# Optimization experiments

Hardware: AMD Instinct MI355X
Metric: run time of the kernel (lower is better)

Reference implementation:

```python
import jax, jax.numpy as jnp
import numpy as np

D_S = 1024
N_HEADS = 16
HEAD_DIM = D_S // N_HEADS
FFN_DIM = 4096
B, S = 2, 1024
LN_EPS = 1e-5


def _layernorm(x, gamma, beta):
    mu = jnp.mean(x, axis=-1, keepdims=True)
    var = jnp.var(x, axis=-1, keepdims=True)
    return (x - mu) * jax.lax.rsqrt(var + LN_EPS) * gamma + beta


def _mish(x):
    return x * jnp.tanh(jax.nn.softplus(x))


def setup_inputs() -> dict:
    key = jax.random.key(0)
    ks = jax.random.split(key, 12)
    std = 1.0 / np.sqrt(D_S)
    return {
        "x": jax.random.normal(ks[0], (B, S, D_S), jnp.float32),
        "attn_bias": jax.random.normal(ks[1], (B, N_HEADS, S, S), jnp.float32),
        "ln1_g": jnp.ones((D_S,), jnp.float32),
        "ln1_b": jnp.zeros((D_S,), jnp.float32),
        "Wqkv": jax.random.normal(ks[2], (D_S, 3 * D_S), jnp.float32) * std,
        "bqkv": jax.random.normal(ks[3], (3 * D_S,), jnp.float32) * 0.02,
        "Wo": jax.random.normal(ks[4], (D_S, D_S), jnp.float32) * std,
        "bo": jax.random.normal(ks[5], (D_S,), jnp.float32) * 0.02,
        "ln2_g": jnp.ones((D_S,), jnp.float32),
        "ln2_b": jnp.zeros((D_S,), jnp.float32),
        "W1": jax.random.normal(ks[6], (D_S, FFN_DIM), jnp.float32) * std,
        "b1": jax.random.normal(ks[7], (FFN_DIM,), jnp.float32) * 0.02,
        "W2": jax.random.normal(ks[8], (FFN_DIM, D_S), jnp.float32) * (1.0 / np.sqrt(FFN_DIM)),
        "b2": jax.random.normal(ks[9], (D_S,), jnp.float32) * 0.02,
    }


def reference(x, attn_bias, ln1_g, ln1_b, Wqkv, bqkv, Wo, bo, ln2_g, ln2_b, W1, b1, W2, b2):
    b, s, d = x.shape
    h = _layernorm(x, ln1_g, ln1_b)
    qkv = (h @ Wqkv + bqkv).reshape(b, s, 3, N_HEADS, HEAD_DIM)
    q, k, v = qkv[:, :, 0], qkv[:, :, 1], qkv[:, :, 2]  # [B,S,H,hd]
    scale = HEAD_DIM ** -0.5
    # scores: [B,H,S,S]
    scores = jnp.einsum("bqhd,bkhd->bhqk", q, k) * scale + attn_bias
    attn = jax.nn.softmax(scores, axis=-1)
    ctx = jnp.einsum("bhqk,bkhd->bqhd", attn, v).reshape(b, s, d)
    x = x + (ctx @ Wo + bo)
    h2 = _layernorm(x, ln2_g, ln2_b)
    ffn = _mish(h2 @ W1 + b1) @ W2 + b2
    return x + ffn
```

## Files before the change

### kernel.cpp

```cpp
#include <hip/hip_runtime.h>


typedef __attribute__((ext_vector_type(8))) __bf16 bf16x8;
typedef __attribute__((ext_vector_type(4))) float  f32x4;

__device__ __forceinline__ unsigned short f2bf(float f) {
  unsigned int u = __builtin_bit_cast(unsigned int, f);
  u += 0x7fffu + ((u >> 16) & 1u);
  return (unsigned short)(u >> 16);
}

__device__ __forceinline__ void gload16(const void* g, void* l) {
  __builtin_amdgcn_global_load_lds(
      (const __attribute__((address_space(1))) void*)g,
      (__attribute__((address_space(3))) void*)l, 16, 0, 0);
}

__global__ void convert_all(const float* __restrict__ Wqkv, const float* __restrict__ Wo,
                            const float* __restrict__ W1, const float* __restrict__ W2,
                            unsigned short* __restrict__ wqkv_t, unsigned short* __restrict__ wo_t,
                            unsigned short* __restrict__ w1_t, unsigned short* __restrict__ w2_t) {
  const int id = blockIdx.x;
  const float* W; unsigned short* Wt; int K, N, t;
  if (id < 3072)      { W = Wqkv; Wt = wqkv_t; K = 1024; N = 3072; t = id; }
  else if (id < 4096) { W = Wo;   Wt = wo_t;   K = 1024; N = 1024; t = id - 3072; }
  else if (id < 8192) { W = W1;   Wt = w1_t;   K = 1024; N = 4096; t = id - 4096; }
  else                { W = W2;   Wt = w2_t;   K = 4096; N = 1024; t = id - 8192; }
  const int nx = N >> 5;
  const int n0 = (t % nx) * 32, k0 = (t / nx) * 32;

  __shared__ float tile[32][33];
  const int tx = threadIdx.x, ty = threadIdx.y;
#pragma unroll
  for (int r = 0; r < 4; ++r)
    tile[ty + 8 * r][tx] = W[(size_t)(k0 + ty + 8 * r) * N + n0 + tx];
  __syncthreads();
#pragma unroll
  for (int r = 0; r < 4; ++r)
    Wt[(size_t)(n0 + ty + 8 * r) * K + k0 + tx] = f2bf(tile[tx][ty + 8 * r]);
}

__global__ __launch_bounds__(256) void ln_kernel(const float* __restrict__ in,
                                                 const float* __restrict__ g,
                                                 const float* __restrict__ b,
                                                 unsigned short* __restrict__ out) {
  const int row = blockIdx.x;
  const int t = threadIdx.x;
  const float4 v = reinterpret_cast<const float4*>(in + (size_t)row * 1024)[t];
  float s  = v.x + v.y + v.z + v.w;
  float s2 = v.x * v.x + v.y * v.y + v.z * v.z + v.w * v.w;
#pragma unroll
  for (int m = 1; m < 64; m <<= 1) { s += __shfl_xor(s, m); s2 += __shfl_xor(s2, m); }
  __shared__ float ps[4], ps2[4];
  const int wv = t >> 6;
  if ((t & 63) == 0) { ps[wv] = s; ps2[wv] = s2; }
  __syncthreads();
  float ts = 0.f, ts2 = 0.f;
#pragma unroll
  for (int i = 0; i < 4; ++i) { ts += ps[i]; ts2 += ps2[i]; }
  const float mu = ts * (1.f / 1024.f);
  const float var = ts2 * (1.f / 1024.f) - mu * mu;
  const float rstd = rsqrtf(var + 1e-5f);
  const float4 gg = reinterpret_cast<const float4*>(g)[t];
  const float4 bb = reinterpret_cast<const float4*>(b)[t];
  ushort4 ov;
  ov.x = f2bf((v.x - mu) * rstd * gg.x + bb.x);
  ov.y = f2bf((v.y - mu) * rstd * gg.y + bb.y);
  ov.z = f2bf((v.z - mu) * rstd * gg.z + bb.z);
  ov.w = f2bf((v.w - mu) * rstd * gg.w + bb.w);
  *reinterpret_cast<ushort4*>(out + (size_t)row * 1024 + t * 4) = ov;
}

template <int MODE, int BM, int BN>
__global__ __launch_bounds__(256, 2) void gemm_kernel(
    const unsigned short* __restrict__ A, const unsigned short* __restrict__ Bt,
    const float* __restrict__ bias, int M, int N, int K,
    float* __restrict__ outf, const float* __restrict__ res,
    unsigned short* __restrict__ outb,
    unsigned short* __restrict__ kbuf, unsigned short* __restrict__ vtbuf) {
  constexpr int BK = 64;
  constexpr int WN = (BN >= 128 || BM == 64) ? 2 : 1;
  constexpr int WM = 4 / WN;
  constexpr int WR = BM / WM / 16;
  constexpr int WC = BN / WN / 16;
  constexpr int AI = BM / 32, BI = BN / 32;
  __shared__ unsigned short a_sh[2][BM * BK];
  __shared__ unsigned short b_sh[2][BN * BK];

  const int tid = threadIdx.x;
  const int wave = tid >> 6, lane = tid & 63;
  const int wm = wave / WN, wn = wave % WN;
  const int l15 = lane & 15, l4 = lane >> 4;

  const int nwg = gridDim.x, cpx = nwg >> 3;
  const int swz = (blockIdx.x & 7) * cpx + (blockIdx.x >> 3);
  const int GY = M / BM;
  const long bm0 = (long)(swz % GY) * BM;
  const long bn0 = (long)(swz / GY) * BN;

  const int sr8 = lane >> 3;
  const int gc  = ((lane & 7) ^ sr8) * 8;

  const unsigned short* agp[AI];
  const unsigned short* bgp[BI];
  int aoff[AI], boff[BI];
#pragma unroll
  for (int i = 0; i < AI; ++i) {
    const int r = wave * (BM / 4) + i * 8;
    agp[i] = A + (bm0 + r + sr8) * (long)K + gc;
    aoff[i] = r * BK;
  }
#pragma unroll
  for (int i = 0; i < BI; ++i) {
    const int r = wave * (BN / 4) + i * 8;
    bgp[i] = Bt + (bn0 + r + sr8) * (long)K + gc;
    boff[i] = r * BK;
  }

  auto stage = [&](int buf, int k0) {
#pragma unroll
    for (int i = 0; i < AI; ++i) gload16(agp[i] + k0, &a_sh[buf][aoff[i]]);
#pragma unroll
    for (int i = 0; i < BI; ++i) gload16(bgp[i] + k0, &b_sh[buf][boff[i]]);
  };

  f32x4 acc[WR][WC] = {};

  stage(0, 0);
  asm volatile("s_waitcnt vmcnt(0)" ::: "memory");
  __syncthreads();

  const int NT = K / BK;
  for (int t = 0; t < NT; ++t) {
    const int cur = t & 1;
    if (t + 1 < NT) stage(cur ^ 1, (t + 1) * BK);

#pragma unroll
    for (int kk = 0; kk < 2; ++kk) {
      bf16x8 af[WR], bfr[WC];
#pragma unroll
      for (int mf = 0; mf < WR; ++mf) {
        const int r = wm * (BM / WM) + mf * 16 + l15;
        const int c = ((kk * 4 + l4) ^ (r & 7)) * 8;
        af[mf] = *reinterpret_cast<const bf16x8*>(&a_sh[cur][r * BK + c]);
      }
#pragma unroll
      for (int nf = 0; nf < WC; ++nf) {
        const int r = wn * (BN / WN) + nf * 16 + l15;
        const int c = ((kk * 4 + l4) ^ (r & 7)) * 8;
        bfr[nf] = *reinterpret_cast<const bf16x8*>(&b_sh[cur][r * BK + c]);
      }
#pragma unroll
      for (int mf = 0; mf < WR; ++mf)
#pragma unroll
        for (int nf = 0; nf < WC; ++nf)
          acc[mf][nf] = __builtin_amdgcn_mfma_f32_16x16x32_bf16(af[mf], bfr[nf], acc[mf][nf], 0, 0, 0);
    }

    asm volatile("s_waitcnt vmcnt(0)" ::: "memory");
    __syncthreads();
  }

#pragma unroll
  for (int mf = 0; mf < WR; ++mf) {
#pragma unroll
    for (int nf = 0; nf < WC; ++nf) {
#pragma unroll
      for (int r = 0; r < 4; ++r) {
        const long row = bm0 + wm * (BM / WM) + mf * 16 + 4 * l4 + r;
        const long col = bn0 + wn * (BN / WN) + nf * 16 + l15;
        float v = acc[mf][nf][r] + bias[col];
        if constexpr (MODE == 0) {
          const int n = (int)col;
          const int which = n >> 10, rem = n & 1023;
          const int head = rem >> 6, d = rem & 63;
          const int b = (int)(row >> 10), s = (int)(row & 1023);
          const unsigned short bv = f2bf(v);
          const long qi = ((long)(b * 16 + head) * 1024 + s) * 64 + d;
          if (which == 0)      outb[qi] = bv;
          else if (which == 1) kbuf[qi] = bv;
          else                 vtbuf[((long)(b * 16 + head) * 64 + d) * 1024 + s] = bv;
        } else if constexpr (MODE == 1) {
          outf[row * N + col] = v + res[row * N + col];
        } else if constexpr (MODE == 2) {
          float mv;
          if (v > 20.f) mv = v;
          else { const float t2 = __expf(v); const float u = t2 * t2 + 2.f * t2;
                 mv = v * u / (u + 2.f); }
          outb[row * (long)N + col] = f2bf(mv);
        } else {
          outf[row * N + col] = v + res[row * N + col];
        }
      }
    }
  }
}

__global__ __launch_bounds__(512, 2) void attn_kernel(
    const unsigned short* __restrict__ qb, const unsigned short* __restrict__ kb,
    const unsigned short* __restrict__ vtb, const float* __restrict__ bias,
    unsigned short* __restrict__ ctx) {
  constexpr int S = 1024;
  __shared__ unsigned short k_sh[2][64 * 64];
  __shared__ unsigned short vt_sh[2][64 * 64];
  __shared__ unsigned short p_sh[8][16 * 72];

  const int bh = blockIdx.y;
  const int q0 = blockIdx.x * 128;
  const int tid = threadIdx.x, wave = tid >> 6, lane = tid & 63;
  const int l15 = lane & 15, l4 = lane >> 4;

  const long qbase = ((long)bh * S + q0 + wave * 16 + l15) * 64;
  const bf16x8 qf0 = *reinterpret_cast<const bf16x8*>(qb + qbase + 8 * l4);
  const bf16x8 qf1 = *reinterpret_cast<const bf16x8*>(qb + qbase + 8 * l4 + 32);

  const int sr8 = lane >> 3;
  const int gchunk = ((lane & 7) ^ sr8) * 8;
  const long kbase = (long)bh * S * 64;
  const long vbase = (long)bh * 64 * S;

  const float* bB = bias + ((long)bh * S + q0 + wave * 16 + 4 * l4) * S + l15;

  f32x4 oacc[4] = {};
  float lacc[4] = {};
  float ba[4][4], bb2[4][4];

  auto stageKV = [&](int kv, int buf) {
    const int r = wave * 8;
    gload16(kb + kbase + (long)(kv + r + sr8) * 64 + gchunk, &k_sh[buf][r * 64]);
    gload16(vtb + vbase + (long)(r + sr8) * S + kv + gchunk, &vt_sh[buf][r * 64]);
  };

  stageKV(0, 0);
#pragma unroll
  for (int r = 0; r < 4; ++r)
#pragma unroll
    for (int nf = 0; nf < 4; ++nf)
      ba[r][nf] = bB[(long)r * S + nf * 16];
  asm volatile("s_waitcnt vmcnt(0)" ::: "memory");
  __syncthreads();

#pragma unroll 1
  for (int tt = 0; tt < 8; ++tt) {
    const int t0 = 2 * tt;
#pragma unroll
    for (int half = 0; half < 2; ++half) {
      const int t = t0 + half;
      const int cur = half, nxt = half ^ 1;
      float (*bcur)[4] = half ? bb2 : ba;
      float (*bnxt)[4] = half ? ba : bb2;

      if (t < 15) stageKV((t + 1) * 64, nxt);

      f32x4 sc[4];
#pragma unroll
      for (int nf = 0; nf < 4; ++nf) {
        const int r = nf * 16 + l15;
        const bf16x8 kf0 = *reinterpret_cast<const bf16x8*>(
            &k_sh[cur][r * 64 + ((l4) ^ (r & 7)) * 8]);
        const bf16x8 kf1 = *reinterpret_cast<const bf16x8*>(
            &k_sh[cur][r * 64 + ((l4 + 4) ^ (r & 7)) * 8]);
        f32x4 z = {};
        z = __builtin_amdgcn_mfma_f32_16x16x32_bf16(qf0, kf0, z, 0, 0, 0);
        sc[nf] = __builtin_amdgcn_mfma_f32_16x16x32_bf16(qf1, kf1, z, 0, 0, 0);
      }

      if (t < 15) {
        const float* bn = bB + (t + 1) * 64;
#pragma unroll
        for (int r = 0; r < 4; ++r)
#pragma unroll
          for (int nf = 0; nf < 4; ++nf)
            bnxt[r][nf] = bn[(long)r * S + nf * 16];
      }

      float pv[4][4];
#pragma unroll
      for (int r = 0; r < 4; ++r) {
        float ls = 0.f;
#pragma unroll
        for (int nf = 0; nf < 4; ++nf) {
          const float p = __expf(sc[nf][r] * 0.125f + bcur[r][nf]);
          pv[nf][r] = p;
          ls += p;
        }
        lacc[r] += ls;
      }

#pragma unroll
      for (int nf = 0; nf < 4; ++nf)
#pragma unroll
        for (int r = 0; r < 4; ++r)
          p_sh[wave][(4 * l4 + r) * 72 + nf * 16 + l15] = f2bf(pv[nf][r]);

      const bf16x8 pa0 = *reinterpret_cast<const bf16x8*>(&p_sh[wave][l15 * 72 + 8 * l4]);
      const bf16x8 pa1 = *reinterpret_cast<const bf16x8*>(&p_sh[wave][l15 * 72 + 8 * l4 + 32]);
#pragma unroll
      for (int nf = 0; nf < 4; ++nf) {
        const int r = nf * 16 + l15;
        const bf16x8 vf0 = *reinterpret_cast<const bf16x8*>(
            &vt_sh[cur][r * 64 + ((l4) ^ (r & 7)) * 8]);
        const bf16x8 vf1 = *reinterpret_cast<const bf16x8*>(
            &vt_sh[cur][r * 64 + ((l4 + 4) ^ (r & 7)) * 8]);
        oacc[nf] = __builtin_amdgcn_mfma_f32_16x16x32_bf16(pa0, vf0, oacc[nf], 0, 0, 0);
        oacc[nf] = __builtin_amdgcn_mfma_f32_16x16x32_bf16(pa1, vf1, oacc[nf], 0, 0, 0);
      }

      asm volatile("s_waitcnt vmcnt(0)" ::: "memory");
      __syncthreads();
    }
  }

#pragma unroll
  for (int r = 0; r < 4; ++r) {
    float v = lacc[r];
    v += __shfl_xor(v, 1);
    v += __shfl_xor(v, 2);
    v += __shfl_xor(v, 4);
    v += __shfl_xor(v, 8);
    lacc[r] = 1.f / v;
  }

  const int b = bh >> 4, h = bh & 15;
#pragma unroll
  for (int nf = 0; nf < 4; ++nf)
#pragma unroll
    for (int r = 0; r < 4; ++r) {
      const long s = q0 + wave * 16 + 4 * l4 + r;
      const long col = h * 64 + nf * 16 + l15;
      ctx[((long)b * S + s) * 1024 + col] = f2bf(oacc[nf][r] * lacc[r]);
    }
}

extern "C" void kernel_launch(void* const* d_in, const int* in_sizes, int n_in,
                              void* d_out, int out_size, void* d_ws, size_t ws_size,
                              hipStream_t stream) {
  const float* x    = (const float*)d_in[0];
  const float* ab   = (const float*)d_in[1];
  const float* ln1g = (const float*)d_in[2];
  const float* ln1b = (const float*)d_in[3];
  const float* Wqkv = (const float*)d_in[4];
  const float* bqkv = (const float*)d_in[5];
  const float* Wo   = (const float*)d_in[6];
  const float* bo   = (const float*)d_in[7];
  const float* ln2g = (const float*)d_in[8];
  const float* ln2b = (const float*)d_in[9];
  const float* W1   = (const float*)d_in[10];
  const float* b1   = (const float*)d_in[11];
  const float* W2   = (const float*)d_in[12];
  const float* b2   = (const float*)d_in[13];
  float* out = (float*)d_out;

  char* ws = (char*)d_ws;
  size_t off = 0;
  auto alloc = [&](size_t bytes) {
    char* p = ws + off;
    off += (bytes + 255) & ~(size_t)255;
    return p;
  };
  unsigned short* wqkv_t = (unsigned short*)alloc((size_t)3072 * 1024 * 2);
  unsigned short* wo_t   = (unsigned short*)alloc((size_t)1024 * 1024 * 2);
  unsigned short* w1_t   = (unsigned short*)alloc((size_t)4096 * 1024 * 2);
  unsigned short* w2_t   = (unsigned short*)alloc((size_t)4096 * 1024 * 2);
  unsigned short* h1     = (unsigned short*)alloc((size_t)2048 * 1024 * 2);
  unsigned short* qbuf   = (unsigned short*)alloc((size_t)2048 * 1024 * 2);
  unsigned short* kbuf   = (unsigned short*)alloc((size_t)2048 * 1024 * 2);
  unsigned short* vtbuf  = (unsigned short*)alloc((size_t)2048 * 1024 * 2);
  unsigned short* ctx    = (unsigned short*)alloc((size_t)2048 * 1024 * 2);
  unsigned short* h2     = (unsigned short*)alloc((size_t)2048 * 1024 * 2);
  float*          r1     = (float*)alloc((size_t)2048 * 1024 * 4);
  unsigned short* ffn1   = h1;
  (void)ws_size; (void)in_sizes; (void)n_in; (void)out_size;

  convert_all<<<12288, dim3(32, 8), 0, stream>>>(Wqkv, Wo, W1, W2,
                                                 wqkv_t, wo_t, w1_t, w2_t);

  ln_kernel<<<2048, 256, 0, stream>>>(x, ln1g, ln1b, h1);

  gemm_kernel<0, 128, 128><<<384, 256, 0, stream>>>(h1, wqkv_t, bqkv, 2048, 3072, 1024,
                                                    nullptr, nullptr, qbuf, kbuf, vtbuf);

  attn_kernel<<<dim3(8, 32), 512, 0, stream>>>(qbuf, kbuf, vtbuf, ab, ctx);

  gemm_kernel<1, 64, 64><<<512, 256, 0, stream>>>(ctx, wo_t, bo, 2048, 1024, 1024,
                                                  r1, x, nullptr, nullptr, nullptr);

  ln_kernel<<<2048, 256, 0, stream>>>(r1, ln2g, ln2b, h2);

  gemm_kernel<2, 128, 128><<<512, 256, 0, stream>>>(h2, w1_t, b1, 2048, 4096, 1024,
                                                    nullptr, nullptr, ffn1, nullptr, nullptr);

  gemm_kernel<3, 64, 64><<<512, 256, 0, stream>>>(ffn1, w2_t, b2, 2048, 1024, 4096,
                                                  out, r1, nullptr, nullptr, nullptr);
}
```

Measured before the change: 178.4 us.

## Triple-buffer GEMM, use 8 waves for 128 tiles, fuse LN1 into convert

New measurement: 193.0 us. +8.2%, slower.

```diff
diff --git a/kernel.cpp b/kernel.cpp
--- a/kernel.cpp
+++ b/kernel.cpp
@@ -16,28 +16,60 @@
       (__attribute__((address_space(3))) void*)l, 16, 0, 0);
 }
 
-__global__ void convert_all(const float* __restrict__ Wqkv, const float* __restrict__ Wo,
-                            const float* __restrict__ W1, const float* __restrict__ W2,
-                            unsigned short* __restrict__ wqkv_t, unsigned short* __restrict__ wo_t,
-                            unsigned short* __restrict__ w1_t, unsigned short* __restrict__ w2_t) {
+__global__ __launch_bounds__(256) void convert_ln(
+    const float* __restrict__ Wqkv, const float* __restrict__ Wo,
+    const float* __restrict__ W1, const float* __restrict__ W2,
+    const float* __restrict__ x, const float* __restrict__ g,
+    const float* __restrict__ bln,
+    unsigned short* __restrict__ wqkv_t, unsigned short* __restrict__ wo_t,
+    unsigned short* __restrict__ w1_t, unsigned short* __restrict__ w2_t,
+    unsigned short* __restrict__ h1) {
+  __shared__ float tile[32][33];
+  __shared__ float ps[4], ps2[4];
   const int id = blockIdx.x;
-  const float* W; unsigned short* Wt; int K, N, t;
-  if (id < 3072)      { W = Wqkv; Wt = wqkv_t; K = 1024; N = 3072; t = id; }
-  else if (id < 4096) { W = Wo;   Wt = wo_t;   K = 1024; N = 1024; t = id - 3072; }
-  else if (id < 8192) { W = W1;   Wt = w1_t;   K = 1024; N = 4096; t = id - 4096; }
-  else                { W = W2;   Wt = w2_t;   K = 4096; N = 1024; t = id - 8192; }
-  const int nx = N >> 5;
-  const int n0 = (t % nx) * 32, k0 = (t / nx) * 32;
-
-  __shared__ float tile[32][33];
   const int tx = threadIdx.x, ty = threadIdx.y;
-#pragma unroll
-  for (int r = 0; r < 4; ++r)
-    tile[ty + 8 * r][tx] = W[(size_t)(k0 + ty + 8 * r) * N + n0 + tx];
-  __syncthreads();
-#pragma unroll
-  for (int r = 0; r < 4; ++r)
-    Wt[(size_t)(n0 + ty + 8 * r) * K + k0 + tx] = f2bf(tile[tx][ty + 8 * r]);
+
+  if (id < 12288) {
+    const float* W; unsigned short* Wt; int K, N, t;
+    if (id < 3072)      { W = Wqkv; Wt = wqkv_t; K = 1024; N = 3072; t = id; }
+    else if (id < 4096) { W = Wo;   Wt = wo_t;   K = 1024; N = 1024; t = id - 3072; }
+    else if (id < 8192) { W = W1;   Wt = w1_t;   K = 1024; N = 4096; t = id - 4096; }
+    else                { W = W2;   Wt = w2_t;   K = 4096; N = 1024; t = id - 8192; }
+    const int nx = N >> 5;
+    const int n0 = (t % nx) * 32, k0 = (t / nx) * 32;
+#pragma unroll
+    for (int r = 0; r < 4; ++r)
+      tile[ty + 8 * r][tx] = W[(size_t)(k0 + ty + 8 * r) * N + n0 + tx];
+    __syncthreads();
+#pragma unroll
+    for (int r = 0; r < 4; ++r)
+      Wt[(size_t)(n0 + ty + 8 * r) * K + k0 + tx] = f2bf(tile[tx][ty + 8 * r]);
+  } else {
+    const int row = id - 12288;
+    const int t = ty * 32 + tx;
+    const float4 v = reinterpret_cast<const float4*>(x + (size_t)row * 1024)[t];
+    float s  = v.x + v.y + v.z + v.w;
+    float s2 = v.x * v.x + v.y * v.y + v.z * v.z + v.w * v.w;
+#pragma unroll
+    for (int m = 1; m < 64; m <<= 1) { s += __shfl_xor(s, m); s2 += __shfl_xor(s2, m); }
+    const int wv = t >> 6;
+    if ((t & 63) == 0) { ps[wv] = s; ps2[wv] = s2; }
+    __syncthreads();
+    float ts = 0.f, ts2 = 0.f;
+#pragma unroll
+    for (int i = 0; i < 4; ++i) { ts += ps[i]; ts2 += ps2[i]; }
+    const float mu = ts * (1.f / 1024.f);
+    const float var = ts2 * (1.f / 1024.f) - mu * mu;
+    const float rstd = rsqrtf(var + 1e-5f);
+    const float4 gg = reinterpret_cast<const float4*>(g)[t];
+    const float4 bb = reinterpret_cast<const float4*>(bln)[t];
+    ushort4 ov;
+    ov.x = f2bf((v.x - mu) * rstd * gg.x + bb.x);
+    ov.y = f2bf((v.y - mu) * rstd * gg.y + bb.y);
+    ov.z = f2bf((v.z - mu) * rstd * gg.z + bb.z);
+    ov.w = f2bf((v.w - mu) * rstd * gg.w + bb.w);
+    *reinterpret_cast<ushort4*>(h1 + (size_t)row * 1024 + t * 4) = ov;
+  }
 }
 
 __global__ __launch_bounds__(256) void ln_kernel(const float* __restrict__ in,
@@ -72,24 +104,24 @@
 }
 
 template <int MODE, int BM, int BN>
-__global__ __launch_bounds__(256, 2) void gemm_kernel(
+__global__ __launch_bounds__(BM == 128 ? 512 : 256, BM == 128 ? 2 : 3)
+void gemm_kernel(
     const unsigned short* __restrict__ A, const unsigned short* __restrict__ Bt,
     const float* __restrict__ bias, int M, int N, int K,
     float* __restrict__ outf, const float* __restrict__ res,
     unsigned short* __restrict__ outb,
     unsigned short* __restrict__ kbuf, unsigned short* __restrict__ vtbuf) {
   constexpr int BK = 64;
-  constexpr int WN = (BN >= 128 || BM == 64) ? 2 : 1;
-  constexpr int WM = 4 / WN;
-  constexpr int WR = BM / WM / 16;
-  constexpr int WC = BN / WN / 16;
-  constexpr int AI = BM / 32, BI = BN / 32;
-  __shared__ unsigned short a_sh[2][BM * BK];
-  __shared__ unsigned short b_sh[2][BN * BK];
+  constexpr int NW  = (BM == 128) ? 8 : 4;
+  constexpr int WNG = NW / 2;
+  constexpr int WR  = BM / 32;
+  constexpr int WC  = 2;
+  __shared__ unsigned short a_sh[3][BM * BK];
+  __shared__ unsigned short b_sh[3][BN * BK];
 
   const int tid = threadIdx.x;
   const int wave = tid >> 6, lane = tid & 63;
-  const int wm = wave / WN, wn = wave % WN;
+  const int wm = wave / WNG, wn = wave % WNG;
   const int l15 = lane & 15, l4 = lane >> 4;
 
   const int nwg = gridDim.x, cpx = nwg >> 3;
@@ -101,52 +133,50 @@
   const int sr8 = lane >> 3;
   const int gc  = ((lane & 7) ^ sr8) * 8;
 
-  const unsigned short* agp[AI];
-  const unsigned short* bgp[BI];
-  int aoff[AI], boff[BI];
-#pragma unroll
-  for (int i = 0; i < AI; ++i) {
-    const int r = wave * (BM / 4) + i * 8;
+  const unsigned short* agp[2];
+  const unsigned short* bgp[2];
+  int aoff[2], boff[2];
+#pragma unroll
+  for (int i = 0; i < 2; ++i) {
+    const int r = (wave * 2 + i) * 8;
     agp[i] = A + (bm0 + r + sr8) * (long)K + gc;
     aoff[i] = r * BK;
-  }
-#pragma unroll
-  for (int i = 0; i < BI; ++i) {
-    const int r = wave * (BN / 4) + i * 8;
     bgp[i] = Bt + (bn0 + r + sr8) * (long)K + gc;
     boff[i] = r * BK;
   }
 
   auto stage = [&](int buf, int k0) {
 #pragma unroll
-    for (int i = 0; i < AI; ++i) gload16(agp[i] + k0, &a_sh[buf][aoff[i]]);
-#pragma unroll
-    for (int i = 0; i < BI; ++i) gload16(bgp[i] + k0, &b_sh[buf][boff[i]]);
+    for (int i = 0; i < 2; ++i) gload16(agp[i] + k0, &a_sh[buf][aoff[i]]);
+#pragma unroll
+    for (int i = 0; i < 2; ++i) gload16(bgp[i] + k0, &b_sh[buf][boff[i]]);
   };
 
   f32x4 acc[WR][WC] = {};
+  const int NT = K / BK;
 
   stage(0, 0);
-  asm volatile("s_waitcnt vmcnt(0)" ::: "memory");
+  stage(1, BK);
+  asm volatile("s_waitcnt vmcnt(4)" ::: "memory");
   __syncthreads();
 
-  const int NT = K / BK;
   for (int t = 0; t < NT; ++t) {
-    const int cur = t & 1;
-    if (t + 1 < NT) stage(cur ^ 1, (t + 1) * BK);
+    const int cur = t % 3;
+    const bool pf = (t + 2 < NT);
+    if (pf) stage((t + 2) % 3, (t + 2) * BK);
 
 #pragma unroll
     for (int kk = 0; kk < 2; ++kk) {
       bf16x8 af[WR], bfr[WC];
 #pragma unroll
       for (int mf = 0; mf < WR; ++mf) {
-        const int r = wm * (BM / WM) + mf * 16 + l15;
+        const int r = wm * (BM / 2) + mf * 16 + l15;
         const int c = ((kk * 4 + l4) ^ (r & 7)) * 8;
         af[mf] = *reinterpret_cast<const bf16x8*>(&a_sh[cur][r * BK + c]);
       }
 #pragma unroll
       for (int nf = 0; nf < WC; ++nf) {
-        const int r = wn * (BN / WN) + nf * 16 + l15;
+        const int r = wn * 32 + nf * 16 + l15;
         const int c = ((kk * 4 + l4) ^ (r & 7)) * 8;
         bfr[nf] = *reinterpret_cast<const bf16x8*>(&b_sh[cur][r * BK + c]);
       }
@@ -157,7 +187,8 @@
           acc[mf][nf] = __builtin_amdgcn_mfma_f32_16x16x32_bf16(af[mf], bfr[nf], acc[mf][nf], 0, 0, 0);
     }
 
-    asm volatile("s_waitcnt vmcnt(0)" ::: "memory");
+    if (pf) asm volatile("s_waitcnt vmcnt(4)" ::: "memory");
+    else    asm volatile("s_waitcnt vmcnt(0)" ::: "memory");
     __syncthreads();
   }
 
@@ -167,8 +198,8 @@
     for (int nf = 0; nf < WC; ++nf) {
 #pragma unroll
       for (int r = 0; r < 4; ++r) {
-        const long row = bm0 + wm * (BM / WM) + mf * 16 + 4 * l4 + r;
-        const long col = bn0 + wn * (BN / WN) + nf * 16 + l15;
+        const long row = bm0 + wm * (BM / 2) + mf * 16 + 4 * l4 + r;
+        const long col = bn0 + wn * 32 + nf * 16 + l15;
         float v = acc[mf][nf][r] + bias[col];
         if constexpr (MODE == 0) {
           const int n = (int)col;
@@ -372,13 +403,11 @@
   unsigned short* ffn1   = h1;
   (void)ws_size; (void)in_sizes; (void)n_in; (void)out_size;
 
-  convert_all<<<12288, dim3(32, 8), 0, stream>>>(Wqkv, Wo, W1, W2,
-                                                 wqkv_t, wo_t, w1_t, w2_t);
-
-  ln_kernel<<<2048, 256, 0, stream>>>(x, ln1g, ln1b, h1);
-
-  gemm_kernel<0, 128, 128><<<384, 256, 0, stream>>>(h1, wqkv_t, bqkv, 2048, 3072, 1024,
-                                                    nullptr, nullptr, qbuf, kbuf, vtbuf);
+  convert_ln<<<14336, dim3(32, 8), 0, stream>>>(Wqkv, Wo, W1, W2, x, ln1g, ln1b,
+                                                wqkv_t, wo_t, w1_t, w2_t, h1);
+
+  gemm_kernel<0, 64, 64><<<1536, 256, 0, stream>>>(h1, wqkv_t, bqkv, 2048, 3072, 1024,
+                                                   nullptr, nullptr, qbuf, kbuf, vtbuf);
 
   attn_kernel<<<dim3(8, 32), 512, 0, stream>>>(qbuf, kbuf, vtbuf, ab, ctx);
 
@@ -387,7 +416,7 @@
 
   ln_kernel<<<2048, 256, 0, stream>>>(r1, ln2g, ln2b, h2);
 
-  gemm_kernel<2, 128, 128><<<512, 256, 0, stream>>>(h2, w1_t, b1, 2048, 4096, 1024,
+  gemm_kernel<2, 128, 128><<<512, 512, 0, stream>>>(h2, w1_t, b1, 2048, 4096, 1024,
                                                     nullptr, nullptr, ffn1, nullptr, nullptr);
 
   gemm_kernel<3, 64, 64><<<512, 256, 0, stream>>>(ffn1, w2_t, b2, 2048, 1024, 4096,
```
